# Optimization experiments

Measured on AMD Instinct MI355X. Metric: run time of the kernel, lower is better.

## Reference

```python
import jax, jax.numpy as jnp
import numpy as np

N_EMB = 8192
D = 512
BETA = 0.25  # commitment_cost, legacy loss: commit + beta*codebook
EPS = 1e-12  # F.normalize eps


def _l2norm(x):
    n = jnp.sqrt(jnp.sum(x * x, axis=-1, keepdims=True))
    return x / jnp.maximum(n, EPS)


def setup_inputs() -> dict:
    key = jax.random.key(0)
    ks = jax.random.split(key, 6)
    z = jax.random.normal(ks[0], (8, 4096, D), dtype=jnp.float32)
    # frozen codebook, init N(0, D^-0.5)
    embedding = jax.random.normal(ks[1], (N_EMB, D), dtype=jnp.float32) * D ** -0.5
    # embedding_proj: Linear(D, D) default torch init
    lim = 1.0 / np.sqrt(D)
    emb_proj_w = jax.random.uniform(ks[2], (D, D), jnp.float32, -lim, lim)
    emb_proj_b = jax.random.uniform(ks[3], (D,), jnp.float32, -lim, lim)
    # z_proj: identity init, zero bias; perturb slightly to make it non-trivial
    z_proj_w = jnp.eye(D, dtype=jnp.float32) + 0.01 * jax.random.normal(ks[4], (D, D), jnp.float32)
    z_proj_b = jnp.zeros((D,), jnp.float32)
    l2_scale = jnp.asarray(10.0, jnp.float32)
    return {"z": z, "embedding": embedding, "emb_proj_w": emb_proj_w,
            "emb_proj_b": emb_proj_b, "z_proj_w": z_proj_w,
            "z_proj_b": z_proj_b, "l2_scale": l2_scale}


def reference(z, embedding, emb_proj_w, emb_proj_b, z_proj_w, z_proj_b, l2_scale):
    B, T, _ = z.shape
    z_flat = z.reshape(-1, D)                              # [BT, D]
    z_proj = z_flat @ z_proj_w.T + z_proj_b                # [BT, D]
    quant_codebook = embedding @ emb_proj_w.T + emb_proj_b  # [N, D]
    # l2-normalized cosine distances (negated similarity)
    z_n = _l2norm(z_proj)
    c_n = _l2norm(quant_codebook)
    distances = -jnp.einsum('bd,nd->bn', z_n, c_n) * l2_scale  # [BT, N]
    idx = jnp.argmin(distances, axis=1)                    # [BT]
    quantized = quant_codebook[idx].reshape(z.shape)       # [B, T, D]
    commit = jnp.mean((jax.lax.stop_gradient(quantized) - z) ** 2)
    codebook = jnp.mean((quantized - jax.lax.stop_gradient(z)) ** 2)
    vq_loss = commit + BETA * codebook                     # legacy=True
    quantized = z + jax.lax.stop_gradient(quantized - z)   # STE
    return quantized, vq_loss, idx.reshape(B, T)
```

## Files before the change

kernel.cpp:

```cpp
#include <hip/hip_runtime.h>
#include <hip/hip_bf16.h>


#define NQ    32768
#define NEMB  8192
#define DD    512

typedef __attribute__((ext_vector_type(8))) short bf16x8;
typedef __attribute__((ext_vector_type(4))) float f32x4;

__device__ __forceinline__ unsigned short f2bf_rne(float f) {
    unsigned u = __float_as_uint(f);
    unsigned r = u + 0x7FFFu + ((u >> 16) & 1u);
    return (unsigned short)(r >> 16);
}
__device__ __forceinline__ float bf2f(unsigned short b) {
    return __uint_as_float(((unsigned)b) << 16);
}

__device__ __forceinline__ void gload16(const void* g, void* l) {
    __builtin_amdgcn_global_load_lds(
        (const __attribute__((address_space(1))) unsigned int*)g,
        (__attribute__((address_space(3))) unsigned int*)l, 16, 0, 0);
}

__global__ __launch_bounds__(256) void k_split(const float* __restrict__ src,
                                               unsigned short* __restrict__ hi,
                                               unsigned short* __restrict__ lo,
                                               int n4) {
    const float4* s4 = (const float4*)src;
    ushort4* h4 = (ushort4*)hi;
    ushort4* l4 = (ushort4*)lo;
    for (int i = blockIdx.x * blockDim.x + threadIdx.x; i < n4; i += gridDim.x * blockDim.x) {
        float4 v = s4[i];
        ushort4 h, l;
        h.x = f2bf_rne(v.x); l.x = f2bf_rne(v.x - bf2f(h.x));
        h.y = f2bf_rne(v.y); l.y = f2bf_rne(v.y - bf2f(h.y));
        h.z = f2bf_rne(v.z); l.z = f2bf_rne(v.z - bf2f(h.z));
        h.w = f2bf_rne(v.w); l.w = f2bf_rne(v.w - bf2f(h.w));
        h4[i] = h;
        l4[i] = l;
    }
}

__global__ __launch_bounds__(256) void k_wtsplit(const float* __restrict__ W,
                                                 unsigned short* __restrict__ thi,
                                                 unsigned short* __restrict__ tlo) {
    __shared__ float t[32][33];
    const int bx = blockIdx.x * 32;
    const int by = blockIdx.y * 32;
    const int c = threadIdx.x & 31, r0 = threadIdx.x >> 5;
    for (int i = 0; i < 4; ++i) {
        int r = r0 + i * 8;
        t[r][c] = W[(size_t)(by + r) * DD + bx + c];
    }
    __syncthreads();
    for (int i = 0; i < 4; ++i) {
        int r = r0 + i * 8;
        float v = t[c][r];
        unsigned short h = f2bf_rne(v);
        thi[(size_t)(bx + r) * DD + by + c] = h;
        tlo[(size_t)(bx + r) * DD + by + c] = f2bf_rne(v - bf2f(h));
    }
}


__global__ __launch_bounds__(256, 3) void k_qc_mfma(const unsigned short* __restrict__ Ah,
                                                    const unsigned short* __restrict__ Al,
                                                    const unsigned short* __restrict__ Bh,
                                                    const unsigned short* __restrict__ Bl,
                                                    const float* __restrict__ bias,
                                                    float* __restrict__ qc,
                                                    unsigned short* __restrict__ qhi,
                                                    unsigned short* __restrict__ qlo) {
    __shared__ unsigned short sAh[128 * 32];
    __shared__ unsigned short sAl[128 * 32];
    __shared__ unsigned short sBh[128 * 32];
    __shared__ unsigned short sBl[128 * 32];

    const int t    = threadIdx.x;
    const int lane = t & 63;
    const int wave = t >> 6;
    const int wm   = wave >> 1;
    const int wn   = wave & 1;
    const int m0   = blockIdx.y * 128;
    const int n0   = blockIdx.x * 128;

    f32x4 acc[4][4];
    for (int i = 0; i < 4; ++i)
        for (int j = 0; j < 4; ++j) acc[i][j] = (f32x4){0.f, 0.f, 0.f, 0.f};

    const int koff = (((lane >> 4) ^ ((lane >> 1) & 3)) << 3);

    for (int kb = 0; kb < DD; kb += 32) {
        for (int r = 0; r < 2; ++r) {
            const int cbase = r * 256 + wave * 64;
            const int c = cbase + lane;
            const int m = c >> 2;
            const int kg = (c & 3) ^ ((m >> 1) & 3);
            const size_t ga = (size_t)(m0 + m) * DD + kb + kg * 8;
            const size_t gb = (size_t)(n0 + m) * DD + kb + kg * 8;
            gload16(Ah + ga, &sAh[cbase * 8]);
            gload16(Al + ga, &sAl[cbase * 8]);
            gload16(Bh + gb, &sBh[cbase * 8]);
            gload16(Bl + gb, &sBl[cbase * 8]);
        }
        __syncthreads();

        bf16x8 afh[4], afl[4], bfh[4], bfl[4];
        const int ar = wm * 64 + (lane & 15);
        const int br = wn * 64 + (lane & 15);
        for (int i = 0; i < 4; ++i) {
            afh[i] = *(const bf16x8*)&sAh[(ar + i * 16) * 32 + koff];
            afl[i] = *(const bf16x8*)&sAl[(ar + i * 16) * 32 + koff];
            bfh[i] = *(const bf16x8*)&sBh[(br + i * 16) * 32 + koff];
            bfl[i] = *(const bf16x8*)&sBl[(br + i * 16) * 32 + koff];
        }
        for (int i = 0; i < 4; ++i)
            for (int j = 0; j < 4; ++j) {
                acc[i][j] = __builtin_amdgcn_mfma_f32_16x16x32_bf16(afh[i], bfh[j], acc[i][j], 0, 0, 0);
                acc[i][j] = __builtin_amdgcn_mfma_f32_16x16x32_bf16(afh[i], bfl[j], acc[i][j], 0, 0, 0);
                acc[i][j] = __builtin_amdgcn_mfma_f32_16x16x32_bf16(afl[i], bfh[j], acc[i][j], 0, 0, 0);
            }
        __syncthreads();
    }

    const int colb = lane & 15;
    const int g    = lane >> 4;
    float bcol[4];
    for (int tn = 0; tn < 4; ++tn) bcol[tn] = bias[n0 + wn * 64 + tn * 16 + colb];
    for (int tm = 0; tm < 4; ++tm) {
        for (int reg = 0; reg < 4; ++reg) {
            int row = m0 + wm * 64 + tm * 16 + g * 4 + reg;
            for (int tn = 0; tn < 4; ++tn) {
                int col = n0 + wn * 64 + tn * 16 + colb;
                float v = acc[tm][tn][reg] + bcol[tn];
                size_t o = (size_t)row * DD + col;
                qc[o] = v;
                unsigned short h = f2bf_rne(v);
                qhi[o] = h;
                qlo[o] = f2bf_rne(v - bf2f(h));
            }
        }
    }
}

__global__ __launch_bounds__(256, 3) void k_e_mfma(const unsigned short* __restrict__ Ah,
                                                   const unsigned short* __restrict__ Al,
                                                   const unsigned short* __restrict__ Bh,
                                                   const unsigned short* __restrict__ Bl,
                                                   const float* __restrict__ rnorm,
                                                   unsigned short* __restrict__ ehi,
                                                   unsigned short* __restrict__ elo) {
    __shared__ unsigned short sAh[128 * 32];
    __shared__ unsigned short sAl[128 * 32];
    __shared__ unsigned short sBh[128 * 32];
    __shared__ unsigned short sBl[128 * 32];

    const int t    = threadIdx.x;
    const int lane = t & 63;
    const int wave = t >> 6;
    const int wm   = wave >> 1;
    const int wn   = wave & 1;
    const int m0   = blockIdx.y * 128;
    const int n0   = blockIdx.x * 128;

    f32x4 acc[4][4];
    for (int i = 0; i < 4; ++i)
        for (int j = 0; j < 4; ++j) acc[i][j] = (f32x4){0.f, 0.f, 0.f, 0.f};

    const int koff = (((lane >> 4) ^ ((lane >> 1) & 3)) << 3);

    for (int kb = 0; kb < DD; kb += 32) {
        for (int r = 0; r < 2; ++r) {
            const int cbase = r * 256 + wave * 64;
            const int c = cbase + lane;
            const int m = c >> 2;
            const int kg = (c & 3) ^ ((m >> 1) & 3);
            const size_t ga = (size_t)(m0 + m) * DD + kb + kg * 8;
            const size_t gb = (size_t)(n0 + m) * DD + kb + kg * 8;
            gload16(Ah + ga, &sAh[cbase * 8]);
            gload16(Al + ga, &sAl[cbase * 8]);
            gload16(Bh + gb, &sBh[cbase * 8]);
            gload16(Bl + gb, &sBl[cbase * 8]);
        }
        __syncthreads();

        bf16x8 afh[4], afl[4], bfh[4], bfl[4];
        const int ar = wm * 64 + (lane & 15);
        const int br = wn * 64 + (lane & 15);
        for (int i = 0; i < 4; ++i) {
            afh[i] = *(const bf16x8*)&sAh[(ar + i * 16) * 32 + koff];
            afl[i] = *(const bf16x8*)&sAl[(ar + i * 16) * 32 + koff];
            bfh[i] = *(const bf16x8*)&sBh[(br + i * 16) * 32 + koff];
            bfl[i] = *(const bf16x8*)&sBl[(br + i * 16) * 32 + koff];
        }
        for (int i = 0; i < 4; ++i)
            for (int j = 0; j < 4; ++j) {
                acc[i][j] = __builtin_amdgcn_mfma_f32_16x16x32_bf16(afh[i], bfh[j], acc[i][j], 0, 0, 0);
                acc[i][j] = __builtin_amdgcn_mfma_f32_16x16x32_bf16(afh[i], bfl[j], acc[i][j], 0, 0, 0);
                acc[i][j] = __builtin_amdgcn_mfma_f32_16x16x32_bf16(afl[i], bfh[j], acc[i][j], 0, 0, 0);
            }
        __syncthreads();
    }

    const int colb = lane & 15;
    const int g    = lane >> 4;
    for (int tm = 0; tm < 4; ++tm) {
        const int rbase = m0 + wm * 64 + tm * 16 + g * 4;
        float4 rn4 = *(const float4*)&rnorm[rbase];
        const float rnv[4] = {rn4.x, rn4.y, rn4.z, rn4.w};
        for (int reg = 0; reg < 4; ++reg) {
            int row = rbase + reg;
            for (int tn = 0; tn < 4; ++tn) {
                int col = n0 + wn * 64 + tn * 16 + colb;
                float v = acc[tm][tn][reg] * rnv[reg];
                size_t o = (size_t)row * DD + col;
                unsigned short h = f2bf_rne(v);
                ehi[o] = h;
                elo[o] = f2bf_rne(v - bf2f(h));
            }
        }
    }
}

__global__ __launch_bounds__(256) void k_norm(const float* __restrict__ qc,
                                              const float* __restrict__ bz,
                                              float* __restrict__ rnorm,
                                              float* __restrict__ tvec) {
    const int n = blockIdx.x;
    const int t = threadIdx.x;
    float ss = 0.f, tb = 0.f;
    for (int d = t; d < DD; d += 256) {
        float v = qc[(size_t)n * DD + d];
        ss += v * v;
        tb += bz[d] * v;
    }
    for (int off = 32; off; off >>= 1) {
        ss += __shfl_down(ss, off);
        tb += __shfl_down(tb, off);
    }
    __shared__ float s1[4], s2[4];
    int wave = t >> 6, lane = t & 63;
    if (lane == 0) { s1[wave] = ss; s2[wave] = tb; }
    __syncthreads();
    if (t == 0) {
        ss = s1[0] + s1[1] + s1[2] + s1[3];
        tb = s2[0] + s2[1] + s2[2] + s2[3];
        float norm = sqrtf(ss);
        float rn = 1.f / fmaxf(norm, 1e-12f);
        rnorm[n] = rn;
        tvec[n] = tb * rn;
    }
}

__global__ __launch_bounds__(256, 3) void k_scores(const unsigned short* __restrict__ Ah,
                                                   const unsigned short* __restrict__ Al,
                                                   const unsigned short* __restrict__ Bh,
                                                   const unsigned short* __restrict__ Bl,
                                                   const float* __restrict__ tvec,
                                                   unsigned long long* __restrict__ table) {
    __shared__ unsigned short sAh[128 * 32];
    __shared__ unsigned short sAl[128 * 32];
    __shared__ unsigned short sBh[128 * 32];
    __shared__ unsigned short sBl[128 * 32];

    const int t    = threadIdx.x;
    const int lane = t & 63;
    const int wave = t >> 6;
    const int wm   = wave >> 1;
    const int wn   = wave & 1;
    const int m0   = blockIdx.y * 128;
    const int n0   = blockIdx.x * 128;

    f32x4 acc[4][4];
    for (int i = 0; i < 4; ++i)
        for (int j = 0; j < 4; ++j) acc[i][j] = (f32x4){0.f, 0.f, 0.f, 0.f};

    const int koff = (((lane >> 4) ^ ((lane >> 1) & 3)) << 3);

    for (int kb = 0; kb < DD; kb += 32) {
        for (int r = 0; r < 2; ++r) {
            const int cbase = r * 256 + wave * 64;
            const int c = cbase + lane;
            const int m = c >> 2;
            const int kg = (c & 3) ^ ((m >> 1) & 3);
            const size_t ga = (size_t)(m0 + m) * DD + kb + kg * 8;
            const size_t gb = (size_t)(n0 + m) * DD + kb + kg * 8;
            gload16(Ah + ga, &sAh[cbase * 8]);
            gload16(Al + ga, &sAl[cbase * 8]);
            gload16(Bh + gb, &sBh[cbase * 8]);
            gload16(Bl + gb, &sBl[cbase * 8]);
        }
        __syncthreads();

        bf16x8 afh[4], afl[4], bfh[4], bfl[4];
        const int ar = wm * 64 + (lane & 15);
        const int br = wn * 64 + (lane & 15);
        for (int i = 0; i < 4; ++i) {
            afh[i] = *(const bf16x8*)&sAh[(ar + i * 16) * 32 + koff];
            afl[i] = *(const bf16x8*)&sAl[(ar + i * 16) * 32 + koff];
            bfh[i] = *(const bf16x8*)&sBh[(br + i * 16) * 32 + koff];
            bfl[i] = *(const bf16x8*)&sBl[(br + i * 16) * 32 + koff];
        }
        for (int i = 0; i < 4; ++i)
            for (int j = 0; j < 4; ++j) {
                acc[i][j] = __builtin_amdgcn_mfma_f32_16x16x32_bf16(afh[i], bfh[j], acc[i][j], 0, 0, 0);
                acc[i][j] = __builtin_amdgcn_mfma_f32_16x16x32_bf16(afh[i], bfl[j], acc[i][j], 0, 0, 0);
                acc[i][j] = __builtin_amdgcn_mfma_f32_16x16x32_bf16(afl[i], bfh[j], acc[i][j], 0, 0, 0);
            }
        __syncthreads();
    }

    const int col = lane & 15;
    const int g   = lane >> 4;
    float tc[4];
    for (int tn = 0; tn < 4; ++tn) tc[tn] = tvec[n0 + wn * 64 + tn * 16 + col];

    for (int tm = 0; tm < 4; ++tm) {
        for (int reg = 0; reg < 4; ++reg) {
            float best = -3.4e38f;
            int   bn   = 0x7FFFFFFF;
            for (int tn = 0; tn < 4; ++tn) {
                float v = acc[tm][tn][reg] + tc[tn];
                int n = n0 + wn * 64 + tn * 16 + col;
                if (v > best || (v == best && n < bn)) { best = v; bn = n; }
            }
            for (int off = 1; off < 16; off <<= 1) {
                float ov = __shfl_xor(best, off);
                int   on = __shfl_xor(bn, off);
                if (ov > best || (ov == best && on < bn)) { best = ov; bn = on; }
            }
            if (col == 0) {
                unsigned u = __float_as_uint(best);
                unsigned key = (u & 0x80000000u) ? ~u : (u | 0x80000000u);
                unsigned long long packed =
                    ((unsigned long long)key << 32) |
                    (unsigned long long)(0xFFFFFFFFu - (unsigned)bn);
                int q = m0 + wm * 64 + tm * 16 + g * 4 + reg;
                atomicMax(&table[q], packed);
            }
        }
    }
}

__global__ __launch_bounds__(128) void k_gather(const unsigned long long* __restrict__ table,
                                                const float* __restrict__ qc,
                                                const float* __restrict__ z,
                                                float* __restrict__ outq,
                                                float* __restrict__ partials,
                                                float* __restrict__ outidx) {
    const int q = blockIdx.x;
    const int t = threadIdx.x;
    unsigned long long p = table[q];
    const int idx = (int)(0xFFFFFFFFu - (unsigned)(p & 0xFFFFFFFFull));
    const float4* src = (const float4*)(qc + (size_t)idx * DD);
    const float4* zs  = (const float4*)(z + (size_t)q * DD);
    float4* dst = (float4*)(outq + (size_t)q * DD);
    float4 a = src[t], b = zs[t];
    dst[t] = a;
    float dx = a.x - b.x, dy = a.y - b.y, dz = a.z - b.z, dw = a.w - b.w;
    float ss = dx * dx + dy * dy + dz * dz + dw * dw;
    for (int off = 32; off; off >>= 1) ss += __shfl_down(ss, off);
    __shared__ float sbuf[2];
    if ((t & 63) == 0) sbuf[t >> 6] = ss;
    __syncthreads();
    if (t == 0) {
        partials[q] = sbuf[0] + sbuf[1];
        outidx[q] = (float)idx;
    }
}

__global__ __launch_bounds__(1024) void k_loss(const float* __restrict__ partials,
                                               float* __restrict__ loss) {
    const int t = threadIdx.x;
    float s = 0.f;
    for (int i = t; i < NQ; i += 1024) s += partials[i];
    for (int off = 32; off; off >>= 1) s += __shfl_down(s, off);
    __shared__ float sbuf[16];
    if ((t & 63) == 0) sbuf[t >> 6] = s;
    __syncthreads();
    if (t == 0) {
        float tot = 0.f;
        for (int w = 0; w < 16; ++w) tot += sbuf[w];
        *loss = tot * (1.25f / 16777216.0f);
    }
}

extern "C" void kernel_launch(void* const* d_in, const int* in_sizes, int n_in,
                              void* d_out, int out_size, void* d_ws, size_t ws_size,
                              hipStream_t stream) {
    (void)in_sizes; (void)n_in; (void)out_size; (void)ws_size;
    const float* z   = (const float*)d_in[0];
    const float* emb = (const float*)d_in[1];
    const float* Wp  = (const float*)d_in[2];
    const float* bp  = (const float*)d_in[3];
    const float* Wz  = (const float*)d_in[4];
    const float* bz  = (const float*)d_in[5];

    float* out = (float*)d_out;
    char* ws = (char*)d_ws;
    float* qc            = (float*)(ws + 0);
    float* rnorm         = (float*)(ws + 16777216);
    float* tvec          = (float*)(ws + 16809984);
    unsigned short* ehi  = (unsigned short*)(ws + 16842752);
    unsigned short* elo  = (unsigned short*)(ws + 25231360);
    unsigned short* zhi  = (unsigned short*)(ws + 33619968);
    unsigned short* zlo  = (unsigned short*)(ws + 67174400);
    unsigned long long* table = (unsigned long long*)(ws + 100728832);

    unsigned short* embhi = (unsigned short*)(ws + 33619968);
    unsigned short* emblo = (unsigned short*)(ws + 33619968 + 8388608);
    unsigned short* qchi  = (unsigned short*)(ws + 33619968 + 16777216);
    unsigned short* qclo  = (unsigned short*)(ws + 33619968 + 25165824);
    unsigned short* wphi  = (unsigned short*)(ws + 67174400);
    unsigned short* wplo  = (unsigned short*)(ws + 67174400 + 524288);
    unsigned short* wzthi = (unsigned short*)(ws + 67174400 + 1048576);
    unsigned short* wztlo = (unsigned short*)(ws + 67174400 + 1572864);
    float* partials      = (float*)(ws + 33619968);

    hipMemsetAsync(table, 0, (size_t)NQ * 8, stream);

    k_split<<<1024, 256, 0, stream>>>(emb, embhi, emblo, NEMB * DD / 4);
    k_split<<<256, 256, 0, stream>>>(Wp, wphi, wplo, DD * DD / 4);
    k_wtsplit<<<dim3(16, 16), 256, 0, stream>>>(Wz, wzthi, wztlo);

    k_qc_mfma<<<dim3(DD / 128, NEMB / 128), 256, 0, stream>>>(embhi, emblo, wphi, wplo,
                                                              bp, qc, qchi, qclo);
    k_norm<<<NEMB, 256, 0, stream>>>(qc, bz, rnorm, tvec);
    k_e_mfma<<<dim3(DD / 128, NEMB / 128), 256, 0, stream>>>(qchi, qclo, wzthi, wztlo,
                                                             rnorm, ehi, elo);
    k_split<<<4096, 256, 0, stream>>>(z, zhi, zlo, NQ * DD / 4);

    k_scores<<<dim3(NEMB / 128, NQ / 128), 256, 0, stream>>>(zhi, zlo, ehi, elo, tvec, table);
    k_gather<<<NQ, 128, 0, stream>>>(table, qc, z,
                                     out,
                                     partials,
                                     out + (size_t)NQ * DD + 1);
    k_loss<<<1, 1024, 0, stream>>>(partials, out + (size_t)NQ * DD);
}
```

Before: 1.007 ms.

## Use single-pass bf16 scoring with exact rescoring of near-best candidates

Replaces the three-term hi/lo bf16 split GEMM for query–codebook scores with a single bf16 hi×hi MFMA pass. Each score is also written as bf16 to a large workspace buffer. A new per-query select kernel re-scores in full split precision only the codes whose approximate score lies within a margin of the approximate max, then does the gather and loss partials. This cuts the dominant GEMM's MFMA work and drops the z lo split. In exchange it adds about half a gigabyte of score writes and reads, and relies on a heuristic margin for correct argmin. The path is gated on the workspace size, so it may not run.

```diff
diff --git a/kernel.cpp b/kernel.cpp
--- a/kernel.cpp
+++ b/kernel.cpp
@@ -43,6 +43,22 @@
     }
 }
 
+__global__ __launch_bounds__(256) void k_split_hi(const float* __restrict__ src,
+                                                  unsigned short* __restrict__ hi,
+                                                  int n4) {
+    const float4* s4 = (const float4*)src;
+    ushort4* h4 = (ushort4*)hi;
+    for (int i = blockIdx.x * blockDim.x + threadIdx.x; i < n4; i += gridDim.x * blockDim.x) {
+        float4 v = s4[i];
+        ushort4 h;
+        h.x = f2bf_rne(v.x);
+        h.y = f2bf_rne(v.y);
+        h.z = f2bf_rne(v.z);
+        h.w = f2bf_rne(v.w);
+        h4[i] = h;
+    }
+}
+
 __global__ __launch_bounds__(256) void k_wtsplit(const float* __restrict__ W,
                                                  unsigned short* __restrict__ thi,
                                                  unsigned short* __restrict__ tlo) {
@@ -252,6 +268,184 @@
         rnorm[n] = rn;
         tvec[n] = tb * rn;
     }
+}
+
+__global__ __launch_bounds__(256, 3) void k_scores1(const unsigned short* __restrict__ Ah,
+                                                    const unsigned short* __restrict__ Bh,
+                                                    const float* __restrict__ tvec,
+                                                    unsigned long long* __restrict__ table,
+                                                    unsigned short* __restrict__ scores) {
+    __shared__ unsigned short sAh[128 * 32];
+    __shared__ unsigned short sBh[128 * 32];
+
+    const int t    = threadIdx.x;
+    const int lane = t & 63;
+    const int wave = t >> 6;
+    const int wm   = wave >> 1;
+    const int wn   = wave & 1;
+    const int m0   = blockIdx.y * 128;
+    const int n0   = blockIdx.x * 128;
+
+    f32x4 acc[4][4];
+    for (int i = 0; i < 4; ++i)
+        for (int j = 0; j < 4; ++j) acc[i][j] = (f32x4){0.f, 0.f, 0.f, 0.f};
+
+    const int koff = (((lane >> 4) ^ ((lane >> 1) & 3)) << 3);
+
+    for (int kb = 0; kb < DD; kb += 32) {
+        for (int r = 0; r < 2; ++r) {
+            const int cbase = r * 256 + wave * 64;
+            const int c = cbase + lane;
+            const int m = c >> 2;
+            const int kg = (c & 3) ^ ((m >> 1) & 3);
+            const size_t ga = (size_t)(m0 + m) * DD + kb + kg * 8;
+            const size_t gb = (size_t)(n0 + m) * DD + kb + kg * 8;
+            gload16(Ah + ga, &sAh[cbase * 8]);
+            gload16(Bh + gb, &sBh[cbase * 8]);
+        }
+        __syncthreads();
+
+        bf16x8 afh[4], bfh[4];
+        const int ar = wm * 64 + (lane & 15);
+        const int br = wn * 64 + (lane & 15);
+        for (int i = 0; i < 4; ++i) {
+            afh[i] = *(const bf16x8*)&sAh[(ar + i * 16) * 32 + koff];
+            bfh[i] = *(const bf16x8*)&sBh[(br + i * 16) * 32 + koff];
+        }
+        for (int i = 0; i < 4; ++i)
+            for (int j = 0; j < 4; ++j)
+                acc[i][j] = __builtin_amdgcn_mfma_f32_16x16x32_bf16(afh[i], bfh[j], acc[i][j], 0, 0, 0);
+        __syncthreads();
+    }
+
+    const int col = lane & 15;
+    const int g   = lane >> 4;
+    float tc[4];
+    for (int tn = 0; tn < 4; ++tn) tc[tn] = tvec[n0 + wn * 64 + tn * 16 + col];
+
+    for (int tm = 0; tm < 4; ++tm) {
+        for (int reg = 0; reg < 4; ++reg) {
+            const int q = m0 + wm * 64 + tm * 16 + g * 4 + reg;
+            float best = -3.4e38f;
+            int   bn   = 0x7FFFFFFF;
+            for (int tn = 0; tn < 4; ++tn) {
+                float v = acc[tm][tn][reg] + tc[tn];
+                int n = n0 + wn * 64 + tn * 16 + col;
+                scores[(size_t)q * NEMB + n] = f2bf_rne(v);
+                if (v > best || (v == best && n < bn)) { best = v; bn = n; }
+            }
+            for (int off = 1; off < 16; off <<= 1) {
+                float ov = __shfl_xor(best, off);
+                int   on = __shfl_xor(bn, off);
+                if (ov > best || (ov == best && on < bn)) { best = ov; bn = on; }
+            }
+            if (col == 0) {
+                unsigned u = __float_as_uint(best);
+                unsigned key = (u & 0x80000000u) ? ~u : (u | 0x80000000u);
+                unsigned long long packed =
+                    ((unsigned long long)key << 32) |
+                    (unsigned long long)(0xFFFFFFFFu - (unsigned)bn);
+                atomicMax(&table[q], packed);
+            }
+        }
+    }
+}
+
+__global__ __launch_bounds__(256) void k_select(const unsigned long long* __restrict__ table,
+                                                const unsigned short* __restrict__ scores,
+                                                const float* __restrict__ z,
+                                                const float* __restrict__ tvec,
+                                                const unsigned short* __restrict__ ehi,
+                                                const unsigned short* __restrict__ elo,
+                                                const float* __restrict__ qc,
+                                                float* __restrict__ outq,
+                                                float* __restrict__ partials,
+                                                float* __restrict__ outidx) {
+    const int q = blockIdx.x;
+    const int t = threadIdx.x;
+    const int lane = t & 63;
+    const int wave = t >> 6;
+    __shared__ float zrow[DD];
+    __shared__ float sred[4];
+    __shared__ unsigned long long sred64[4];
+    __shared__ int sidx;
+
+    float zz = 0.f;
+    for (int d = t; d < DD; d += 256) {
+        float v = z[(size_t)q * DD + d];
+        zrow[d] = v;
+        zz += v * v;
+    }
+    for (int off = 32; off; off >>= 1) zz += __shfl_down(zz, off);
+    if (lane == 0) sred[wave] = zz;
+    __syncthreads();
+    const float znorm = sqrtf(sred[0] + sred[1] + sred[2] + sred[3]);
+
+    unsigned long long p = table[q];
+    unsigned key = (unsigned)(p >> 32);
+    float maxv = (key & 0x80000000u) ? __uint_as_float(key & 0x7FFFFFFFu)
+                                     : __uint_as_float(~key);
+    const float thr = maxv - (0.02f * znorm + 0.01f * (fabsf(maxv) + 1.0f));
+
+    float bbest = -3.4e38f;
+    int   bbn   = 0x7FFFFFFF;
+    const unsigned short* srow = scores + (size_t)q * NEMB + t * 32;
+    for (int c = 0; c < 4; ++c) {
+        ushort4 u0 = *(const ushort4*)(srow + c * 8);
+        ushort4 u1 = *(const ushort4*)(srow + c * 8 + 4);
+        const unsigned short uu[8] = {u0.x, u0.y, u0.z, u0.w, u1.x, u1.y, u1.z, u1.w};
+        for (int e = 0; e < 8; ++e) {
+            if (bf2f(uu[e]) >= thr) {
+                const int n = t * 32 + c * 8 + e;
+                float s = tvec[n];
+                const ushort4* eh = (const ushort4*)(ehi + (size_t)n * DD);
+                const ushort4* el = (const ushort4*)(elo + (size_t)n * DD);
+                for (int d4 = 0; d4 < DD / 4; ++d4) {
+                    ushort4 h = eh[d4], l = el[d4];
+                    s += zrow[d4 * 4 + 0] * (bf2f(h.x) + bf2f(l.x));
+                    s += zrow[d4 * 4 + 1] * (bf2f(h.y) + bf2f(l.y));
+                    s += zrow[d4 * 4 + 2] * (bf2f(h.z) + bf2f(l.z));
+                    s += zrow[d4 * 4 + 3] * (bf2f(h.w) + bf2f(l.w));
+                }
+                if (s > bbest || (s == bbest && n < bbn)) { bbest = s; bbn = n; }
+            }
+        }
+    }
+    unsigned bu = __float_as_uint(bbest);
+    unsigned bk = (bu & 0x80000000u) ? ~bu : (bu | 0x80000000u);
+    unsigned long long pk = ((unsigned long long)bk << 32) |
+                            (unsigned long long)(0xFFFFFFFFu - (unsigned)bbn);
+    for (int off = 32; off; off >>= 1) {
+        unsigned long long o = __shfl_down(pk, off);
+        if (o > pk) pk = o;
+    }
+    if (lane == 0) sred64[wave] = pk;
+    __syncthreads();
+    if (t == 0) {
+        unsigned long long m = sred64[0];
+        for (int w = 1; w < 4; ++w) if (sred64[w] > m) m = sred64[w];
+        int idx = (int)(0xFFFFFFFFu - (unsigned)(m & 0xFFFFFFFFull));
+        sidx = idx;
+        outidx[q] = (float)idx;
+    }
+    __syncthreads();
+    const int idx = sidx;
+
+    float ss = 0.f;
+    if (t < 128) {
+        float4 a = *(const float4*)(qc + (size_t)idx * DD + t * 4);
+        *(float4*)(outq + (size_t)q * DD + t * 4) = a;
+        float d0 = a.x - zrow[t * 4 + 0];
+        float d1 = a.y - zrow[t * 4 + 1];
+        float d2 = a.z - zrow[t * 4 + 2];
+        float d3 = a.w - zrow[t * 4 + 3];
+        ss = d0 * d0 + d1 * d1 + d2 * d2 + d3 * d3;
+    }
+    for (int off = 32; off; off >>= 1) ss += __shfl_down(ss, off);
+    __syncthreads();
+    if (lane == 0) sred[wave] = ss;
+    __syncthreads();
+    if (t == 0) partials[q] = sred[0] + sred[1] + sred[2] + sred[3];
 }
 
 __global__ __launch_bounds__(256, 3) void k_scores(const unsigned short* __restrict__ Ah,
@@ -390,7 +584,7 @@
 extern "C" void kernel_launch(void* const* d_in, const int* in_sizes, int n_in,
                               void* d_out, int out_size, void* d_ws, size_t ws_size,
                               hipStream_t stream) {
-    (void)in_sizes; (void)n_in; (void)out_size; (void)ws_size;
+    (void)in_sizes; (void)n_in; (void)out_size;
     const float* z   = (const float*)d_in[0];
     const float* emb = (const float*)d_in[1];
     const float* Wp  = (const float*)d_in[2];
@@ -408,6 +602,7 @@
     unsigned short* zhi  = (unsigned short*)(ws + 33619968);
     unsigned short* zlo  = (unsigned short*)(ws + 67174400);
     unsigned long long* table = (unsigned long long*)(ws + 100728832);
+    unsigned short* scores    = (unsigned short*)(ws + 100990976);
 
     unsigned short* embhi = (unsigned short*)(ws + 33619968);
     unsigned short* emblo = (unsigned short*)(ws + 33619968 + 8388608);
@@ -419,6 +614,8 @@
     unsigned short* wztlo = (unsigned short*)(ws + 67174400 + 1572864);
     float* partials      = (float*)(ws + 33619968);
 
+    const bool fast = ws_size >= 637861888ull;
+
     hipMemsetAsync(table, 0, (size_t)NQ * 8, stream);
 
     k_split<<<1024, 256, 0, stream>>>(emb, embhi, emblo, NEMB * DD / 4);
@@ -430,12 +627,16 @@
     k_norm<<<NEMB, 256, 0, stream>>>(qc, bz, rnorm, tvec);
     k_e_mfma<<<dim3(DD / 128, NEMB / 128), 256, 0, stream>>>(qchi, qclo, wzthi, wztlo,
                                                              rnorm, ehi, elo);
-    k_split<<<4096, 256, 0, stream>>>(z, zhi, zlo, NQ * DD / 4);
-
-    k_scores<<<dim3(NEMB / 128, NQ / 128), 256, 0, stream>>>(zhi, zlo, ehi, elo, tvec, table);
-    k_gather<<<NQ, 128, 0, stream>>>(table, qc, z,
-                                     out,
-                                     partials,
-                                     out + (size_t)NQ * DD + 1);
+    if (fast) {
+        k_split_hi<<<4096, 256, 0, stream>>>(z, zhi, NQ * DD / 4);
+        k_scores1<<<dim3(NEMB / 128, NQ / 128), 256, 0, stream>>>(zhi, ehi, tvec, table, scores);
+        k_select<<<NQ, 256, 0, stream>>>(table, scores, z, tvec, ehi, elo, qc,
+                                         out, partials, out + (size_t)NQ * DD + 1);
+    } else {
+        k_split<<<4096, 256, 0, stream>>>(z, zhi, zlo, NQ * DD / 4);
+        k_scores<<<dim3(NEMB / 128, NQ / 128), 256, 0, stream>>>(zhi, zlo, ehi, elo, tvec, table);
+        k_gather<<<NQ, 128, 0, stream>>>(table, qc, z, out, partials,
+                                         out + (size_t)NQ * DD + 1);
+    }
     k_loss<<<1, 1024, 0, stream>>>(partials, out + (size_t)NQ * DD);
 }
```

Result: slower. 1.032 ms (+2.5%).
